# Kernel tuning notes

Hardware: AMD Instinct MI355X
Metric: run time of the kernel (lower is better)

The kernel has to match this reference:

```python
import jax, jax.numpy as jnp
import numpy as np

D_HEAD = 64

def setup_inputs() -> dict:
    key = jax.random.key(0)
    kq, kk, kv, km = jax.random.split(key, 4)
    B, H, S, D = 4, 16, 2048, D_HEAD
    q = jax.random.normal(kq, (B, H, S, D), dtype=jnp.float32)
    k = jax.random.normal(kk, (B, H, S, D), dtype=jnp.float32)
    v = jax.random.normal(kv, (B, H, S, D), dtype=jnp.float32)
    mask = jax.random.randint(km, (B, 1, S, S), 0, 2, dtype=jnp.int32)
    return {"q": q, "k": k, "v": v, "mask": mask}

def reference(q, k, v, mask):
    # scores: [B,H,S,S]
    scores = jnp.einsum('bhqd,bhkd->bhqk', q, k) / jnp.sqrt(jnp.asarray(D_HEAD, q.dtype))
    neg_inf = jnp.asarray(-jnp.inf, scores.dtype)
    scores = jnp.where(mask == 0, neg_inf, scores)
    attn = jax.nn.softmax(scores, axis=-1)
    # dropout is identity in eval mode (deterministic reference)
    return jnp.einsum('bhqk,bhkd->bhqd', attn, v)
```

## Files before the change

### kernel.cpp

```cpp
#include <hip/hip_runtime.h>


constexpr int Bc = 4, Hc = 16, Sc = 2048, Dc = 64;
constexpr int QBLK = 128, KVBLK = 64;
constexpr int NT = Sc / KVBLK;

typedef _Float16 half8 __attribute__((ext_vector_type(8)));
typedef _Float16 half4 __attribute__((ext_vector_type(4)));
typedef __fp16  fp16x2 __attribute__((ext_vector_type(2)));
typedef float floatx4 __attribute__((ext_vector_type(4)));

#define GLB(p) ((const __attribute__((address_space(1))) void*)(p))
#define LDSP(p) ((__attribute__((address_space(3))) void*)(p))

union U32F2 { unsigned int u; fp16x2 h; };
union PFRAG { unsigned int u[4]; half8 h; };

__global__ __launch_bounds__(256) void mask_to_bits(
    const int* __restrict__ M, unsigned long long* __restrict__ W)
{
    size_t i = (size_t)blockIdx.x * 256 + threadIdx.x;
    int v = M[i];
    unsigned long long bal = __ballot(v != 0);
    if ((threadIdx.x & 63) == 0) W[i >> 6] = bal;
}

__global__ __launch_bounds__(256) void mask_to_bytes(
    const int* __restrict__ M, unsigned int* __restrict__ M8)
{
    size_t t = (size_t)blockIdx.x * 256 + threadIdx.x;
    const int4* src = (const int4*)M + t * 4;
    uint4 out;
    unsigned int* o = (unsigned int*)&out;
    #pragma unroll
    for (int w = 0; w < 4; ++w) {
        int4 v = src[w];
        o[w] = (v.x ? 0xFFu : 0u) | (v.y ? 0xFF00u : 0u) |
               (v.z ? 0xFF0000u : 0u) | (v.w ? 0xFF000000u : 0u);
    }
    ((uint4*)M8)[t] = out;
}

__global__ __launch_bounds__(256) void kv_convert_v4(
    const float* __restrict__ Kp, const float* __restrict__ Vp,
    unsigned char* __restrict__ K16, unsigned char* __restrict__ V16)
{
    __shared__ float vlds[64][65];
    const int tid = threadIdx.x;
    const int kt  = blockIdx.x;
    const int bh  = blockIdx.y;
    const int kv0 = kt * 64;
    const float* ksrc = Kp + ((size_t)bh * Sc + kv0) * Dc;
    const float* vsrc = Vp + ((size_t)bh * Sc + kv0) * Dc;
    unsigned char* kdst = K16 + (size_t)bh * Sc * 128 + (size_t)kv0 * 128;
    unsigned char* vdst = V16 + (size_t)bh * Sc * 128 + (size_t)kv0 * 128;

    #pragma unroll
    for (int it = 0; it < 4; ++it) {
        int idx = it * 256 + tid;
        int o   = idx >> 4;
        int d0  = (idx & 15) * 4;
        float4 kval = *(const float4*)(ksrc + o * Dc + d0);
        half4 kh;
        kh[0] = (_Float16)kval.x; kh[1] = (_Float16)kval.y;
        kh[2] = (_Float16)kval.z; kh[3] = (_Float16)kval.w;
        int r = ((o >> 2) & 3) * 16 + ((o >> 4) << 2) + (o & 3);
        *(half4*)(kdst + r * 128 + ((d0 * 2) ^ ((r & 7) << 4))) = kh;

        float4 vval = *(const float4*)(vsrc + o * Dc + d0);
        vlds[o][d0]     = vval.x;
        vlds[o][d0 + 1] = vval.y;
        vlds[o][d0 + 2] = vval.z;
        vlds[o][d0 + 3] = vval.w;
    }
    __syncthreads();
    #pragma unroll
    for (int i = 0; i < 2; ++i) {
        int ch  = i * 256 + tid;
        int l15 = ch & 15;
        int lg  = (ch >> 4) & 3;
        int c   = (ch >> 6) & 1;
        int nd  = ch >> 7;
        int d   = nd * 16 + l15;
        half8 h;
        #pragma unroll
        for (int w = 0; w < 4; ++w) {
            int kvlog = lg * 16 + (2 * c + (w >> 1)) * 4 + (w & 1) * 2;
            h[w * 2]     = (_Float16)vlds[kvlog][d];
            h[w * 2 + 1] = (_Float16)vlds[kvlog + 1][d];
        }
        *(half8*)(vdst + ch * 16) = h;
    }
}

template <int MMODE>
__global__ __launch_bounds__(256) void attn_v8(
    const float* __restrict__ Qp,
    const unsigned char* __restrict__ K16, const unsigned char* __restrict__ V16,
    const unsigned char* __restrict__ M8, const unsigned long long* __restrict__ Wb,
    float* __restrict__ Op)
{
    __shared__ __align__(16) unsigned char lds[49152];

    const int tid  = threadIdx.x;
    const int w    = tid >> 6;
    const int lane = tid & 63;
    const int l15  = lane & 15;
    const int lg   = lane >> 4;

    const int ib      = blockIdx.x;
    const int logical = (ib & 7) * 128 + (ib >> 3);
    const int qt = logical & 15;
    const int bh = logical >> 4;
    const int b  = bh >> 4;
    const int q0 = qt * QBLK + w * 32 + l15;
    const int q1 = q0 + 16;

    const size_t qkv_base = (size_t)bh * Sc * Dc;
    const unsigned char* k16src = K16 + (size_t)bh * Sc * 128;
    const unsigned char* v16src = V16 + (size_t)bh * Sc * 128;
    const unsigned char* mp0 = M8 + (size_t)b * Sc * Sc + (size_t)q0 * Sc + lg * 16;
    const unsigned char* mp1 = mp0 + (size_t)16 * Sc;
    const unsigned long long* wr0 = Wb + ((size_t)b * Sc + q0) * (Sc / 64);
    const unsigned long long* wr1 = Wb + ((size_t)b * Sc + q1) * (Sc / 64);

    const float qscale = 0.125f * 1.44269504088896f;
    half8 qfrag[2][2];
    #pragma unroll
    for (int qg = 0; qg < 2; ++qg) {
        const float* qrow = Qp + qkv_base + (size_t)(qg ? q1 : q0) * Dc;
        #pragma unroll
        for (int c = 0; c < 2; ++c) {
            int d0 = c * 32 + lg * 8;
            float4 qa = *(const float4*)(qrow + d0);
            float4 qb = *(const float4*)(qrow + d0 + 4);
            qfrag[qg][c][0] = (_Float16)(qa.x * qscale);
            qfrag[qg][c][1] = (_Float16)(qa.y * qscale);
            qfrag[qg][c][2] = (_Float16)(qa.z * qscale);
            qfrag[qg][c][3] = (_Float16)(qa.w * qscale);
            qfrag[qg][c][4] = (_Float16)(qb.x * qscale);
            qfrag[qg][c][5] = (_Float16)(qb.y * qscale);
            qfrag[qg][c][6] = (_Float16)(qb.z * qscale);
            qfrag[qg][c][7] = (_Float16)(qb.w * qscale);
        }
    }

    half8 ones;
    #pragma unroll
    for (int e = 0; e < 8; ++e) ones[e] = (_Float16)1.0f;

    floatx4 o_acc[2][4];
    floatx4 o_l[2];
    #pragma unroll
    for (int qg = 0; qg < 2; ++qg) {
        o_l[qg] = (floatx4)0.f;
        #pragma unroll
        for (int n = 0; n < 4; ++n) o_acc[qg][n] = (floatx4)0.f;
    }

    const int ldsOff = (w * 2) * 1024;
    const unsigned char* kg = k16src + ldsOff + lane * 16;
    const unsigned char* vg = v16src + ldsOff + lane * 16;

    uint4 mk[3][2];
    unsigned long long wk[3][2];

    auto STAGE = [&](int slot) {
        __builtin_amdgcn_global_load_lds(GLB(kg),        LDSP(lds + slot * 16384 + ldsOff),               16, 0, 0);
        __builtin_amdgcn_global_load_lds(GLB(kg + 1024), LDSP(lds + slot * 16384 + ldsOff + 1024),        16, 0, 0);
        __builtin_amdgcn_global_load_lds(GLB(vg),        LDSP(lds + slot * 16384 + 8192 + ldsOff),        16, 0, 0);
        __builtin_amdgcn_global_load_lds(GLB(vg + 1024), LDSP(lds + slot * 16384 + 8192 + ldsOff + 1024), 16, 0, 0);
        kg += 8192; vg += 8192;
    };
    auto LOADM = [&](int slot) {
        if (MMODE == 0) {
            mk[slot][0] = *(const uint4*)(mp0); mp0 += KVBLK;
            mk[slot][1] = *(const uint4*)(mp1); mp1 += KVBLK;
        } else {
            wk[slot][0] = *wr0; ++wr0;
            wk[slot][1] = *wr1; ++wr1;
        }
    };

    auto COMP = [&](int j) {
        const unsigned char* kbase = lds + j * 16384;
        const unsigned char* vbase = lds + j * 16384 + 8192;

        floatx4 s[2][4];
        __builtin_amdgcn_s_setprio(1);
        #pragma unroll
        for (int n = 0; n < 4; ++n) {
            const unsigned char* krow = kbase + (n * 16 + l15) * 128;
            half8 kf0 = *(const half8*)(krow + ((lg * 16)      ^ ((l15 & 7) << 4)));
            half8 kf1 = *(const half8*)(krow + ((64 + lg * 16) ^ ((l15 & 7) << 4)));
            floatx4 a0 = __builtin_amdgcn_mfma_f32_16x16x32_f16(kf0, qfrag[0][0], (floatx4)0.f, 0, 0, 0);
            a0 = __builtin_amdgcn_mfma_f32_16x16x32_f16(kf1, qfrag[0][1], a0, 0, 0, 0);
            floatx4 a1 = __builtin_amdgcn_mfma_f32_16x16x32_f16(kf0, qfrag[1][0], (floatx4)0.f, 0, 0, 0);
            a1 = __builtin_amdgcn_mfma_f32_16x16x32_f16(kf1, qfrag[1][1], a1, 0, 0, 0);
            s[0][n] = a0;
            s[1][n] = a1;
        }
        __builtin_amdgcn_s_setprio(0);

        PFRAG pf[2][2];
        #pragma unroll
        for (int qg = 0; qg < 2; ++qg) {
            unsigned int nib16;
            if (MMODE == 1) {
                unsigned long long wc = wk[j][qg];
                unsigned int lo = (unsigned int)wc, hi = (unsigned int)(wc >> 32);
                unsigned int half = (lg & 2) ? hi : lo;
                nib16 = (lg & 1) ? (half >> 16) : (half & 0xFFFFu);
            }
            const unsigned int* mw = (const unsigned int*)&mk[j][qg];
            #pragma unroll
            for (int n = 0; n < 4; ++n) {
                float p0 = __builtin_amdgcn_exp2f(s[qg][n][0]);
                float p1 = __builtin_amdgcn_exp2f(s[qg][n][1]);
                float p2 = __builtin_amdgcn_exp2f(s[qg][n][2]);
                float p3 = __builtin_amdgcn_exp2f(s[qg][n][3]);
                U32F2 h01, h23;
                h01.h = __builtin_amdgcn_cvt_pkrtz(p0, p1);
                h23.h = __builtin_amdgcn_cvt_pkrtz(p2, p3);
                unsigned int msk0, msk1;
                if (MMODE == 0) {
                    msk0 = __builtin_amdgcn_perm(0u, mw[n], 0x01010000u);
                    msk1 = __builtin_amdgcn_perm(0u, mw[n], 0x03030202u);
                } else {
                    unsigned int x0 = nib16 >> (n * 4);
                    unsigned int x1 = nib16 >> (n * 4 + 2);
                    msk0 = ((x0 & 1u) | ((x0 & 2u) << 15)) * 0xFFFFu;
                    msk1 = ((x1 & 1u) | ((x1 & 2u) << 15)) * 0xFFFFu;
                }
                pf[qg][n >> 1].u[(n & 1) * 2]     = h01.u & msk0;
                pf[qg][n >> 1].u[(n & 1) * 2 + 1] = h23.u & msk1;
            }
        }

        __builtin_amdgcn_s_setprio(1);
        #pragma unroll
        for (int nd = 0; nd < 4; ++nd) {
            const unsigned char* vrow = vbase + ((nd * 8 + lg) * 16 + l15) * 16;
            half8 vf0 = *(const half8*)(vrow);
            half8 vf1 = *(const half8*)(vrow + 1024);
            o_acc[0][nd] = __builtin_amdgcn_mfma_f32_16x16x32_f16(vf0, pf[0][0].h, o_acc[0][nd], 0, 0, 0);
            o_acc[0][nd] = __builtin_amdgcn_mfma_f32_16x16x32_f16(vf1, pf[0][1].h, o_acc[0][nd], 0, 0, 0);
            o_acc[1][nd] = __builtin_amdgcn_mfma_f32_16x16x32_f16(vf0, pf[1][0].h, o_acc[1][nd], 0, 0, 0);
            o_acc[1][nd] = __builtin_amdgcn_mfma_f32_16x16x32_f16(vf1, pf[1][1].h, o_acc[1][nd], 0, 0, 0);
        }
        #pragma unroll
        for (int qg = 0; qg < 2; ++qg) {
            o_l[qg] = __builtin_amdgcn_mfma_f32_16x16x32_f16(ones, pf[qg][0].h, o_l[qg], 0, 0, 0);
            o_l[qg] = __builtin_amdgcn_mfma_f32_16x16x32_f16(ones, pf[qg][1].h, o_l[qg], 0, 0, 0);
        }
        __builtin_amdgcn_s_setprio(0);
    };

    STAGE(0); LOADM(0);
    STAGE(1); LOADM(1);

    for (int i = 0; i < 10; ++i) {
        #pragma unroll
        for (int j = 0; j < 3; ++j) {
            asm volatile("s_waitcnt vmcnt(6)" ::: "memory");
            __builtin_amdgcn_s_barrier();
            STAGE((j + 2) % 3);
            LOADM((j + 2) % 3);
            COMP(j);
        }
    }
    asm volatile("s_waitcnt vmcnt(6)" ::: "memory");
    __builtin_amdgcn_s_barrier();
    COMP(0);
    asm volatile("s_waitcnt vmcnt(0)" ::: "memory");
    __builtin_amdgcn_s_barrier();
    COMP(1);

    #pragma unroll
    for (int qg = 0; qg < 2; ++qg) {
        float inv_l = 1.0f / o_l[qg][0];
        float* orow = Op + qkv_base + (size_t)(qg ? q1 : q0) * Dc;
        #pragma unroll
        for (int nd = 0; nd < 4; ++nd) {
            float4 st;
            st.x = o_acc[qg][nd][0] * inv_l;
            st.y = o_acc[qg][nd][1] * inv_l;
            st.z = o_acc[qg][nd][2] * inv_l;
            st.w = o_acc[qg][nd][3] * inv_l;
            *(float4*)(orow + nd * 16 + lg * 4) = st;
        }
    }
}

template <bool USE_BITS>
__global__ __launch_bounds__(256) void attn_old(
    const float* __restrict__ Qp, const float* __restrict__ Kp,
    const float* __restrict__ Vp, const int* __restrict__ Mp,
    const unsigned long long* __restrict__ Wb, float* __restrict__ Op)
{
    __shared__ __align__(16) unsigned char lds[24576];
    const int tid  = threadIdx.x;
    const int w    = tid >> 6;
    const int lane = tid & 63;
    const int l15  = lane & 15;
    const int lg   = lane >> 4;
    const int qt = blockIdx.x;
    const int bh = blockIdx.y;
    const int b  = bh >> 4;
    const int qbase = qt * 64;
    const size_t qkv_base = (size_t)bh * Sc * Dc;
    const int*   mrow     = Mp + (size_t)b * Sc * Sc;
    const unsigned long long* wrow =
        Wb + ((size_t)b * Sc + qbase + w * 16 + lg * 4) * (Sc / 64);

    const float qscale = 0.125f * 1.44269504088896f;
    half8 qfrag[2];
    {
        const float* qrow = Qp + qkv_base + (size_t)(qbase + w * 16 + l15) * Dc;
        #pragma unroll
        for (int c = 0; c < 2; ++c) {
            int d0 = c * 32 + lg * 8;
            float4 qa = *(const float4*)(qrow + d0);
            float4 qb = *(const float4*)(qrow + d0 + 4);
            #pragma unroll
            for (int e = 0; e < 4; ++e) qfrag[c][e] = (_Float16)(((const float*)&qa)[e] * qscale);
            #pragma unroll
            for (int e = 0; e < 4; ++e) qfrag[c][4 + e] = (_Float16)(((const float*)&qb)[e] * qscale);
        }
    }
    float m_run[4], l_run[4];
    floatx4 o_acc[4];
    #pragma unroll
    for (int j = 0; j < 4; ++j) { m_run[j] = -1e30f; l_run[j] = 0.f; }
    #pragma unroll
    for (int n = 0; n < 4; ++n) o_acc[n] = (floatx4)0.f;

    for (int kv0 = 0; kv0 < Sc; kv0 += 64) {
        __syncthreads();
        {
            const float* ksrc = Kp + qkv_base + (size_t)kv0 * Dc;
            const float* vsrc = Vp + qkv_base + (size_t)kv0 * Dc;
            #pragma unroll
            for (int it = 0; it < 4; ++it) {
                int idx = it * 256 + tid;
                int kv  = idx >> 4;
                int d0  = (idx & 15) * 4;
                float4 kval = *(const float4*)(ksrc + kv * Dc + d0);
                half4 kh;
                kh[0] = (_Float16)kval.x; kh[1] = (_Float16)kval.y;
                kh[2] = (_Float16)kval.z; kh[3] = (_Float16)kval.w;
                *(half4*)(lds + ((kv * 128 + d0 * 2) ^ ((kv & 7) << 4))) = kh;
                float4 vval = *(const float4*)(vsrc + kv * Dc + d0);
                float vv[4] = { vval.x, vval.y, vval.z, vval.w };
                #pragma unroll
                for (int i = 0; i < 4; ++i) {
                    int d = d0 + i;
                    *(_Float16*)(lds + 8192 + ((d * 128 + kv * 2) ^ ((d & 7) << 4))) = (_Float16)vv[i];
                }
            }
        }
        __syncthreads();

        unsigned int mlo[4], mhi[4];
        if (USE_BITS) {
            #pragma unroll
            for (int j = 0; j < 4; ++j) {
                unsigned long long mw = wrow[(size_t)j * (Sc / 64) + (kv0 >> 6)];
                mlo[j] = (unsigned int)mw;
                mhi[j] = (unsigned int)(mw >> 32);
            }
        }
        floatx4 s[4];
        #pragma unroll
        for (int n = 0; n < 4; ++n) {
            floatx4 acc = (floatx4)0.f;
            #pragma unroll
            for (int c = 0; c < 2; ++c) {
                int kvr = n * 16 + l15;
                int d0  = c * 32 + lg * 8;
                half8 bfrag = *(const half8*)(lds + ((kvr * 128 + d0 * 2) ^ ((kvr & 7) << 4)));
                acc = __builtin_amdgcn_mfma_f32_16x16x32_f16(qfrag[c], bfrag, acc, 0, 0, 0);
            }
            s[n] = acc;
        }
        float tmax[4];
        #pragma unroll
        for (int j = 0; j < 4; ++j) tmax[j] = -1e30f;
        #pragma unroll
        for (int n = 0; n < 4; ++n) {
            #pragma unroll
            for (int j = 0; j < 4; ++j) {
                unsigned int bit;
                if (USE_BITS) {
                    unsigned int word = (n < 2) ? mlo[j] : mhi[j];
                    bit = (word >> (((n & 1) << 4) + l15)) & 1u;
                } else {
                    int qr  = qbase + w * 16 + lg * 4 + j;
                    int kvc = kv0 + n * 16 + l15;
                    bit = (mrow[(size_t)qr * Sc + kvc] != 0) ? 1u : 0u;
                }
                float sv = bit ? s[n][j] : -1e30f;
                s[n][j] = sv;
                tmax[j] = fmaxf(tmax[j], sv);
            }
        }
        #pragma unroll
        for (int j = 0; j < 4; ++j) {
            float tv = tmax[j];
            tv = fmaxf(tv, __shfl_xor(tv, 1));
            tv = fmaxf(tv, __shfl_xor(tv, 2));
            tv = fmaxf(tv, __shfl_xor(tv, 4));
            tv = fmaxf(tv, __shfl_xor(tv, 8));
            tmax[j] = tv;
        }
        float corr[4], rsum[4];
        #pragma unroll
        for (int j = 0; j < 4; ++j) {
            float mnew = fmaxf(m_run[j], tmax[j]);
            corr[j] = exp2f(m_run[j] - mnew);
            m_run[j] = mnew;
            rsum[j] = 0.f;
        }
        unsigned char* pbase = lds + 16384 + w * 2048;
        #pragma unroll
        for (int n = 0; n < 4; ++n) {
            #pragma unroll
            for (int j = 0; j < 4; ++j) {
                float p = exp2f(s[n][j] - m_run[j]);
                rsum[j] += p;
                int off = ((lg * 4 + j) * 128 + (n * 16 + l15) * 2) ^ (((lg * 4 + j) & 7) << 4);
                *(_Float16*)(pbase + off) = (_Float16)p;
            }
        }
        #pragma unroll
        for (int j = 0; j < 4; ++j) {
            float r = rsum[j];
            r += __shfl_xor(r, 1);
            r += __shfl_xor(r, 2);
            r += __shfl_xor(r, 4);
            r += __shfl_xor(r, 8);
            l_run[j] = l_run[j] * corr[j] + r;
        }
        #pragma unroll
        for (int n = 0; n < 4; ++n)
            #pragma unroll
            for (int j = 0; j < 4; ++j)
                o_acc[n][j] *= corr[j];

        half8 pfrag[2];
        #pragma unroll
        for (int c = 0; c < 2; ++c) {
            int kvc = c * 32 + lg * 8;
            pfrag[c] = *(const half8*)(pbase + ((l15 * 128 + kvc * 2) ^ ((l15 & 7) << 4)));
        }
        #pragma unroll
        for (int n = 0; n < 4; ++n) {
            #pragma unroll
            for (int c = 0; c < 2; ++c) {
                int d   = n * 16 + l15;
                int kvc = c * 32 + lg * 8;
                half8 vfrag = *(const half8*)(lds + 8192 + ((d * 128 + kvc * 2) ^ ((d & 7) << 4)));
                o_acc[n] = __builtin_amdgcn_mfma_f32_16x16x32_f16(pfrag[c], vfrag, o_acc[n], 0, 0, 0);
            }
        }
    }
    float inv_l[4];
    #pragma unroll
    for (int j = 0; j < 4; ++j) inv_l[j] = 1.0f / l_run[j];
    float* obase = Op + qkv_base;
    #pragma unroll
    for (int n = 0; n < 4; ++n)
        #pragma unroll
        for (int j = 0; j < 4; ++j)
            obase[(size_t)(qbase + w * 16 + lg * 4 + j) * Dc + n * 16 + l15] = o_acc[n][j] * inv_l[j];
}

extern "C" void kernel_launch(void* const* d_in, const int* in_sizes, int n_in,
                              void* d_out, int out_size, void* d_ws, size_t ws_size,
                              hipStream_t stream) {
    const float* Q = (const float*)d_in[0];
    const float* K = (const float*)d_in[1];
    const float* V = (const float*)d_in[2];
    const int*   M = (const int*)d_in[3];
    float*       O = (float*)d_out;

    const int nblk = (Sc / QBLK) * Bc * Hc;
    const size_t SZ_BITS = (size_t)Bc * Sc * (Sc / 64) * 8;
    const size_t SZ_K    = (size_t)Bc * Hc * Sc * 128;
    const size_t SZ_V    = SZ_K;
    const size_t SZ_M8   = (size_t)Bc * Sc * Sc;

    if (ws_size >= SZ_K + SZ_V + SZ_M8) {
        unsigned char* K16 = (unsigned char*)d_ws;
        unsigned char* V16 = K16 + SZ_K;
        unsigned char* M8  = V16 + SZ_V;
        mask_to_bytes<<<(Bc * Sc * Sc) / (256 * 16), 256, 0, stream>>>(M, (unsigned int*)M8);
        kv_convert_v4<<<dim3(Sc / 64, Bc * Hc), 256, 0, stream>>>(K, V, K16, V16);
        attn_v8<0><<<nblk, 256, 0, stream>>>(Q, K16, V16, M8, nullptr, O);
    } else if (ws_size >= SZ_BITS + SZ_K + SZ_V) {
        unsigned long long* W = (unsigned long long*)d_ws;
        unsigned char* K16 = (unsigned char*)d_ws + SZ_BITS;
        unsigned char* V16 = K16 + SZ_K;
        mask_to_bits<<<(Bc * Sc * Sc) / 256, 256, 0, stream>>>(M, W);
        kv_convert_v4<<<dim3(Sc / 64, Bc * Hc), 256, 0, stream>>>(K, V, K16, V16);
        attn_v8<1><<<nblk, 256, 0, stream>>>(Q, K16, V16, nullptr, W, O);
    } else if (ws_size >= SZ_BITS) {
        unsigned long long* W = (unsigned long long*)d_ws;
        mask_to_bits<<<(Bc * Sc * Sc) / 256, 256, 0, stream>>>(M, W);
        attn_old<true><<<dim3(Sc / 64, Bc * Hc), 256, 0, stream>>>(Q, K, V, M, W, O);
    } else {
        attn_old<false><<<dim3(Sc / 64, Bc * Hc), 256, 0, stream>>>(Q, K, V, M, nullptr, O);
    }
}
```

Before: 123.6 us.

## Use 512-thread blocks with 256-row Q tiles and VALU row-sum

Doubles the Q tile per block to 256 rows with 8 waves, so each K/V tile staged in LDS is shared by twice as many query rows. Each wave now issues half as many global-to-LDS loads, and the vmcnt waits are adjusted to match. The softmax denominator moves from extra MFMAs against a ones vector to VALU fdot2 accumulation plus a final cross-lane shuffle reduction. This trades MFMA work for VALU work and raises register pressure through launch_bounds(512,4).

```diff
diff --git a/kernel.cpp b/kernel.cpp
--- a/kernel.cpp
+++ b/kernel.cpp
@@ -2,11 +2,12 @@
 
 
 constexpr int Bc = 4, Hc = 16, Sc = 2048, Dc = 64;
-constexpr int QBLK = 128, KVBLK = 64;
+constexpr int QBLK = 256, KVBLK = 64;
 constexpr int NT = Sc / KVBLK;
 
 typedef _Float16 half8 __attribute__((ext_vector_type(8)));
 typedef _Float16 half4 __attribute__((ext_vector_type(4)));
+typedef _Float16 half2v __attribute__((ext_vector_type(2)));
 typedef __fp16  fp16x2 __attribute__((ext_vector_type(2)));
 typedef float floatx4 __attribute__((ext_vector_type(4)));
 
@@ -14,7 +15,19 @@
 #define LDSP(p) ((__attribute__((address_space(3))) void*)(p))
 
 union U32F2 { unsigned int u; fp16x2 h; };
+union U32H2 { unsigned int u; half2v h; };
 union PFRAG { unsigned int u[4]; half8 h; };
+
+__device__ inline float dot2acc(unsigned int pu, float acc) {
+#if __has_builtin(__builtin_amdgcn_fdot2)
+    U32H2 c; c.u = pu;
+    half2v ones2 = { (_Float16)1.0f, (_Float16)1.0f };
+    return __builtin_amdgcn_fdot2(c.h, ones2, acc, false);
+#else
+    U32H2 c; c.u = pu;
+    return acc + (float)c.h[0] + (float)c.h[1];
+#endif
+}
 
 __global__ __launch_bounds__(256) void mask_to_bits(
     const int* __restrict__ M, unsigned long long* __restrict__ W)
@@ -94,7 +107,7 @@
 }
 
 template <int MMODE>
-__global__ __launch_bounds__(256) void attn_v8(
+__global__ __launch_bounds__(512, 4) void attn_v9(
     const float* __restrict__ Qp,
     const unsigned char* __restrict__ K16, const unsigned char* __restrict__ V16,
     const unsigned char* __restrict__ M8, const unsigned long long* __restrict__ Wb,
@@ -109,9 +122,9 @@
     const int lg   = lane >> 4;
 
     const int ib      = blockIdx.x;
-    const int logical = (ib & 7) * 128 + (ib >> 3);
-    const int qt = logical & 15;
-    const int bh = logical >> 4;
+    const int logical = (ib & 7) * 64 + (ib >> 3);
+    const int qt = logical & 7;
+    const int bh = logical >> 3;
     const int b  = bh >> 4;
     const int q0 = qt * QBLK + w * 32 + l15;
     const int q1 = q0 + 16;
@@ -145,20 +158,14 @@
         }
     }
 
-    half8 ones;
-    #pragma unroll
-    for (int e = 0; e < 8; ++e) ones[e] = (_Float16)1.0f;
-
     floatx4 o_acc[2][4];
-    floatx4 o_l[2];
-    #pragma unroll
-    for (int qg = 0; qg < 2; ++qg) {
-        o_l[qg] = (floatx4)0.f;
+    float   l_run[2] = {0.f, 0.f};
+    #pragma unroll
+    for (int qg = 0; qg < 2; ++qg)
         #pragma unroll
         for (int n = 0; n < 4; ++n) o_acc[qg][n] = (floatx4)0.f;
-    }
-
-    const int ldsOff = (w * 2) * 1024;
+
+    const int ldsOff = w * 1024;
     const unsigned char* kg = k16src + ldsOff + lane * 16;
     const unsigned char* vg = v16src + ldsOff + lane * 16;
 
@@ -166,10 +173,8 @@
     unsigned long long wk[3][2];
 
     auto STAGE = [&](int slot) {
-        __builtin_amdgcn_global_load_lds(GLB(kg),        LDSP(lds + slot * 16384 + ldsOff),               16, 0, 0);
-        __builtin_amdgcn_global_load_lds(GLB(kg + 1024), LDSP(lds + slot * 16384 + ldsOff + 1024),        16, 0, 0);
-        __builtin_amdgcn_global_load_lds(GLB(vg),        LDSP(lds + slot * 16384 + 8192 + ldsOff),        16, 0, 0);
-        __builtin_amdgcn_global_load_lds(GLB(vg + 1024), LDSP(lds + slot * 16384 + 8192 + ldsOff + 1024), 16, 0, 0);
+        __builtin_amdgcn_global_load_lds(GLB(kg), LDSP(lds + slot * 16384 + ldsOff),        16, 0, 0);
+        __builtin_amdgcn_global_load_lds(GLB(vg), LDSP(lds + slot * 16384 + 8192 + ldsOff), 16, 0, 0);
         kg += 8192; vg += 8192;
     };
     auto LOADM = [&](int slot) {
@@ -213,6 +218,7 @@
                 nib16 = (lg & 1) ? (half >> 16) : (half & 0xFFFFu);
             }
             const unsigned int* mw = (const unsigned int*)&mk[j][qg];
+            float rs = l_run[qg];
             #pragma unroll
             for (int n = 0; n < 4; ++n) {
                 float p0 = __builtin_amdgcn_exp2f(s[qg][n][0]);
@@ -232,9 +238,14 @@
                     msk0 = ((x0 & 1u) | ((x0 & 2u) << 15)) * 0xFFFFu;
                     msk1 = ((x1 & 1u) | ((x1 & 2u) << 15)) * 0xFFFFu;
                 }
-                pf[qg][n >> 1].u[(n & 1) * 2]     = h01.u & msk0;
-                pf[qg][n >> 1].u[(n & 1) * 2 + 1] = h23.u & msk1;
-            }
+                unsigned int w0 = h01.u & msk0;
+                unsigned int w1 = h23.u & msk1;
+                pf[qg][n >> 1].u[(n & 1) * 2]     = w0;
+                pf[qg][n >> 1].u[(n & 1) * 2 + 1] = w1;
+                rs = dot2acc(w0, rs);
+                rs = dot2acc(w1, rs);
+            }
+            l_run[qg] = rs;
         }
 
         __builtin_amdgcn_s_setprio(1);
@@ -248,11 +259,6 @@
             o_acc[1][nd] = __builtin_amdgcn_mfma_f32_16x16x32_f16(vf0, pf[1][0].h, o_acc[1][nd], 0, 0, 0);
             o_acc[1][nd] = __builtin_amdgcn_mfma_f32_16x16x32_f16(vf1, pf[1][1].h, o_acc[1][nd], 0, 0, 0);
         }
-        #pragma unroll
-        for (int qg = 0; qg < 2; ++qg) {
-            o_l[qg] = __builtin_amdgcn_mfma_f32_16x16x32_f16(ones, pf[qg][0].h, o_l[qg], 0, 0, 0);
-            o_l[qg] = __builtin_amdgcn_mfma_f32_16x16x32_f16(ones, pf[qg][1].h, o_l[qg], 0, 0, 0);
-        }
         __builtin_amdgcn_s_setprio(0);
     };
 
@@ -262,14 +268,14 @@
     for (int i = 0; i < 10; ++i) {
         #pragma unroll
         for (int j = 0; j < 3; ++j) {
-            asm volatile("s_waitcnt vmcnt(6)" ::: "memory");
+            asm volatile("s_waitcnt vmcnt(4)" ::: "memory");
             __builtin_amdgcn_s_barrier();
             STAGE((j + 2) % 3);
             LOADM((j + 2) % 3);
             COMP(j);
         }
     }
-    asm volatile("s_waitcnt vmcnt(6)" ::: "memory");
+    asm volatile("s_waitcnt vmcnt(4)" ::: "memory");
     __builtin_amdgcn_s_barrier();
     COMP(0);
     asm volatile("s_waitcnt vmcnt(0)" ::: "memory");
@@ -278,7 +284,10 @@
 
     #pragma unroll
     for (int qg = 0; qg < 2; ++qg) {
-        float inv_l = 1.0f / o_l[qg][0];
+        float r = l_run[qg];
+        r += __shfl_xor(r, 16);
+        r += __shfl_xor(r, 32);
+        float inv_l = 1.0f / r;
         float* orow = Op + qkv_base + (size_t)(qg ? q1 : q0) * Dc;
         #pragma unroll
         for (int nd = 0; nd < 4; ++nd) {
@@ -496,14 +505,14 @@
         unsigned char* M8  = V16 + SZ_V;
         mask_to_bytes<<<(Bc * Sc * Sc) / (256 * 16), 256, 0, stream>>>(M, (unsigned int*)M8);
         kv_convert_v4<<<dim3(Sc / 64, Bc * Hc), 256, 0, stream>>>(K, V, K16, V16);
-        attn_v8<0><<<nblk, 256, 0, stream>>>(Q, K16, V16, M8, nullptr, O);
+        attn_v9<0><<<nblk, 512, 0, stream>>>(Q, K16, V16, M8, nullptr, O);
     } else if (ws_size >= SZ_BITS + SZ_K + SZ_V) {
         unsigned long long* W = (unsigned long long*)d_ws;
         unsigned char* K16 = (unsigned char*)d_ws + SZ_BITS;
         unsigned char* V16 = K16 + SZ_K;
         mask_to_bits<<<(Bc * Sc * Sc) / 256, 256, 0, stream>>>(M, W);
         kv_convert_v4<<<dim3(Sc / 64, Bc * Hc), 256, 0, stream>>>(K, V, K16, V16);
-        attn_v8<1><<<nblk, 256, 0, stream>>>(Q, K16, V16, nullptr, W, O);
+        attn_v9<1><<<nblk, 512, 0, stream>>>(Q, K16, V16, nullptr, W, O);
     } else if (ws_size >= SZ_BITS) {
         unsigned long long* W = (unsigned long long*)d_ws;
         mask_to_bits<<<(Bc * Sc * Sc) / 256, 256, 0, stream>>>(M, W);
```

Result: slower. 165.1 us (+33.5%).
